# Kernel tuning notes

Measured on AMD Instinct MI355X. Metric: run time of the kernel, lower is better.

Reference implementation:

```python
import jax, jax.numpy as jnp
import numpy as np
import math

B, S, D, H = 2, 2048, 2048, 16
HD = D // H  # 128


def setup_inputs() -> dict:
    key = jax.random.key(0)
    ks = jax.random.split(key, 6)
    x = jax.random.normal(ks[0], (B, S, D), dtype=jnp.float32)
    scale = 1.0 / math.sqrt(D)
    wq = jax.random.normal(ks[1], (D, D), dtype=jnp.float32) * scale
    wk = jax.random.normal(ks[2], (D, D), dtype=jnp.float32) * scale
    wv = jax.random.normal(ks[3], (D, D), dtype=jnp.float32) * scale
    wo = jax.random.normal(ks[4], (D, D), dtype=jnp.float32) * scale
    # rotary frequencies: freqs_cis[t, j] = exp(i * t / theta^(2j/HD))
    theta = 10000.0
    inv = 1.0 / (theta ** (jnp.arange(0, HD, 2, dtype=jnp.float32) / HD))  # [HD//2]
    ang = jnp.arange(S, dtype=jnp.float32)[:, None] * inv[None, :]  # [S, HD//2]
    freqs_cos = jnp.cos(ang)
    freqs_sin = jnp.sin(ang)
    # causal additive mask
    mask = jnp.where(jnp.tril(jnp.ones((S, S), dtype=bool)), 0.0, -1e9)
    mask = mask[None, None, :, :].astype(jnp.float32)
    return {"x": x, "wq": wq, "wk": wk, "wv": wv, "wo": wo,
            "freqs_cos": freqs_cos, "freqs_sin": freqs_sin, "mask": mask}


def _rope(t, cos, sin):
    # t: [B, S, H, HD]; cos/sin: [S, HD//2]
    b, s, h, d = t.shape
    t2 = t.reshape(b, s, h, d // 2, 2)
    re, im = t2[..., 0], t2[..., 1]
    c = cos[None, :, None, :]
    sn = sin[None, :, None, :]
    out_re = re * c - im * sn
    out_im = re * sn + im * c
    return jnp.stack([out_re, out_im], axis=-1).reshape(b, s, h, d)


def reference(x, wq, wk, wv, wo, freqs_cos, freqs_sin, mask):
    b, s, _ = x.shape
    xq = (x @ wq.T).reshape(b, s, H, HD)
    xk = (x @ wk.T).reshape(b, s, H, HD)
    xv = (x @ wv.T).reshape(b, s, H, HD)
    xq = _rope(xq, freqs_cos, freqs_sin)
    xk = _rope(xk, freqs_cos, freqs_sin)
    # [B, H, S, HD]
    q = xq.transpose(0, 2, 1, 3)
    k = xk.transpose(0, 2, 1, 3)
    v = xv.transpose(0, 2, 1, 3)
    scores = jnp.einsum("bhqd,bhkd->bhqk", q, k) / math.sqrt(HD)
    scores = scores + mask
    probs = jax.nn.softmax(scores.astype(jnp.float32), axis=-1).astype(q.dtype)
    out = jnp.einsum("bhqk,bhkd->bhqd", probs, v)
    out = out.transpose(0, 2, 1, 3).reshape(b, s, -1)
    return out @ wo.T
```

## Files before the change

### kernel.cpp

```cpp
#include <hip/hip_runtime.h>
#include <math.h>

#define BATCH 2
#define SEQ 2048
#define DMODEL 2048
#define NH 16
#define HD 128

typedef __bf16 bf16x8 __attribute__((ext_vector_type(8)));
typedef __bf16 bf16x4 __attribute__((ext_vector_type(4)));
typedef float f32x4 __attribute__((ext_vector_type(4)));
typedef float f32x16 __attribute__((ext_vector_type(16)));

#define GLL16(dst, src)                                                          \
  __builtin_amdgcn_global_load_lds(                                              \
      (const __attribute__((address_space(1))) void*)(src),                      \
      (__attribute__((address_space(3))) void*)(dst), 16, 0, 0)

__global__ __launch_bounds__(256) void split_fp32(const float* __restrict__ src,
                                                  __bf16* __restrict__ hi,
                                                  __bf16* __restrict__ lo) {
  const size_t i = (size_t)blockIdx.x * 256 + threadIdx.x;
  const float4 v = ((const float4*)src)[i];
  bf16x4 h, L;
  h[0] = (__bf16)v.x; h[1] = (__bf16)v.y; h[2] = (__bf16)v.z; h[3] = (__bf16)v.w;
  L[0] = (__bf16)(v.x - (float)h[0]);
  L[1] = (__bf16)(v.y - (float)h[1]);
  L[2] = (__bf16)(v.z - (float)h[2]);
  L[3] = (__bf16)(v.w - (float)h[3]);
  ((bf16x4*)hi)[i] = h;
  ((bf16x4*)lo)[i] = L;
}

template <int EMIT>
__global__ __launch_bounds__(512, 2) void gemm8(const __bf16* __restrict__ Ah,
                                                const __bf16* __restrict__ Al,
                                                const __bf16* __restrict__ Bh,
                                                const __bf16* __restrict__ Bl,
                                                void* __restrict__ Cout) {
  extern __shared__ char sm[];
  constexpr int NT = 96;
  const int tid = threadIdx.x;
  const int l = tid & 63, w = tid >> 6;
  const int lg = l >> 4, lm = l & 15;
  const int wr = w >> 1, wc = w & 1;

  const int bid = (int)blockIdx.x;
  const int X = bid & 7, sub = bid >> 3;
  const int mb = (X & 3) * 4 + (sub >> 3);
  const int nb = (X >> 2) * 8 + (sub & 7);
  const int m0 = mb * 256, n0 = nb * 128;

  const __bf16* segA[3] = {Ah, Al, Ah};
  const __bf16* segB[3] = {Bh, Bh, Bl};

  const int srow = l >> 3;
  const int co = ((l & 7) ^ srow) * 8;

  char* const Abuf = sm;
  char* const Bbuf = sm + 98304;

  auto stageB = [&](int tb) {
    char* bd = Bbuf + (tb & 1) * 16384;
    const __bf16* sb = segB[tb >> 5];
    const int kw = (tb & 31) * 64;
#pragma unroll
    for (int j = 0; j < 2; ++j)
      GLL16(bd + (w * 2 + j) * 1024,
            sb + (size_t)(n0 + (w * 2 + j) * 8 + srow) * 2048 + kw + co);
  };
  auto stageAu = [&](int ta, int slot, int u) {
    char* ad = Abuf + slot * 32768 + u * 16384;
    const __bf16* sa = segA[ta >> 5];
    const int kw = (ta & 31) * 64;
#pragma unroll
    for (int j = 0; j < 2; ++j)
      GLL16(ad + (w * 2 + j) * 1024,
            sa + (size_t)(m0 + u * 128 + (w * 2 + j) * 8 + srow) * 2048 + kw + co);
  };

  stageAu(0, 0, 0); stageAu(0, 0, 1);
  stageB(0);
  stageAu(1, 1, 0); stageAu(1, 1, 1);

  f32x4 acc[4][4];
#pragma unroll
  for (int i = 0; i < 4; ++i)
#pragma unroll
    for (int j = 0; j < 4; ++j) { f32x4 z = {0.f, 0.f, 0.f, 0.f}; acc[i][j] = z; }

  int sA = 0, sA2 = 2;
  const int swz = lm & 7;

  for (int t = 0; t < NT; ++t) {
    if (t + 1 < NT) { asm volatile("s_waitcnt vmcnt(4)" ::: "memory"); }
    else            { asm volatile("s_waitcnt vmcnt(0)" ::: "memory"); }
    __builtin_amdgcn_sched_barrier(0);
    __builtin_amdgcn_s_barrier();

    const char* Ab = Abuf + sA * 32768;
    const char* Bb = Bbuf + (t & 1) * 16384;
    bf16x8 a[4], b[4];

#pragma unroll
    for (int j = 0; j < 4; ++j)
      b[j] = *(const bf16x8*)(Bb + (wc * 64 + j * 16 + lm) * 128 + ((lg ^ swz) << 4));
#pragma unroll
    for (int i = 0; i < 4; ++i)
      a[i] = *(const bf16x8*)(Ab + (wr * 64 + i * 16 + lm) * 128 + ((lg ^ swz) << 4));
    if (t + 1 < NT) stageB(t + 1);
    if (t + 2 < NT) stageAu(t + 2, sA2, 0);
    __builtin_amdgcn_s_barrier();
    __builtin_amdgcn_s_setprio(1);
#pragma unroll
    for (int i = 0; i < 4; ++i)
#pragma unroll
      for (int j = 0; j < 4; ++j)
        acc[i][j] = __builtin_amdgcn_mfma_f32_16x16x32_bf16(a[i], b[j], acc[i][j], 0, 0, 0);
    __builtin_amdgcn_s_setprio(0);

#pragma unroll
    for (int j = 0; j < 4; ++j)
      b[j] = *(const bf16x8*)(Bb + (wc * 64 + j * 16 + lm) * 128 + (((4 + lg) ^ swz) << 4));
#pragma unroll
    for (int i = 0; i < 4; ++i)
      a[i] = *(const bf16x8*)(Ab + (wr * 64 + i * 16 + lm) * 128 + (((4 + lg) ^ swz) << 4));
    if (t + 2 < NT) stageAu(t + 2, sA2, 1);
    __builtin_amdgcn_s_barrier();
    __builtin_amdgcn_s_setprio(1);
#pragma unroll
    for (int i = 0; i < 4; ++i)
#pragma unroll
      for (int j = 0; j < 4; ++j)
        acc[i][j] = __builtin_amdgcn_mfma_f32_16x16x32_bf16(a[i], b[j], acc[i][j], 0, 0, 0);
    __builtin_amdgcn_s_setprio(0);

    sA = (sA == 2) ? 0 : sA + 1;
    sA2 = (sA2 == 2) ? 0 : sA2 + 1;
  }

#pragma unroll
  for (int i = 0; i < 4; ++i)
#pragma unroll
    for (int j = 0; j < 4; ++j)
#pragma unroll
      for (int r = 0; r < 4; ++r) {
        const size_t row = (size_t)(m0 + wr * 64 + i * 16 + lg * 4 + r);
        const size_t col = (size_t)(n0 + wc * 64 + j * 16 + lm);
        if (EMIT == 0) ((float*)Cout)[row * 2048 + col] = acc[i][j][r];
        else           ((__bf16*)Cout)[row * 2048 + col] = (__bf16)acc[i][j][r];
      }
}

__global__ __launch_bounds__(256) void rope_bf16(__bf16* __restrict__ q,
                                                 __bf16* __restrict__ k,
                                                 const float* __restrict__ cosp,
                                                 const float* __restrict__ sinp) {
  __bf16* t = blockIdx.y ? k : q;
  const float scale = blockIdx.y ? 1.0f : 0.08838834764831845f;
  const size_t i4 = (size_t)blockIdx.x * 256 + threadIdx.x;
  const size_t e = i4 * 4;
  const int srow = (int)((e >> 11) & 2047);
  const int p = (int)(e & 127) >> 1;
  bf16x4 vv = *(bf16x4*)(t + e);
  const float c0 = cosp[srow * 64 + p],     s0 = sinp[srow * 64 + p];
  const float c1 = cosp[srow * 64 + p + 1], s1 = sinp[srow * 64 + p + 1];
  const float re0 = (float)vv[0], im0 = (float)vv[1];
  const float re1 = (float)vv[2], im1 = (float)vv[3];
  bf16x4 o;
  o[0] = (__bf16)((re0 * c0 - im0 * s0) * scale);
  o[1] = (__bf16)((re0 * s0 + im0 * c0) * scale);
  o[2] = (__bf16)((re1 * c1 - im1 * s1) * scale);
  o[3] = (__bf16)((re1 * s1 + im1 * c1) * scale);
  *(bf16x4*)(t + e) = o;
}

static __device__ __forceinline__ unsigned pk2(float a, float b) {
  unsigned short x = __builtin_bit_cast(unsigned short, (__bf16)a);
  unsigned short y = __builtin_bit_cast(unsigned short, (__bf16)b);
  return ((unsigned)y << 16) | (unsigned)x;
}

__global__ __launch_bounds__(256) void attn_mfma2(const __bf16* __restrict__ q,
                                                  const __bf16* __restrict__ k,
                                                  const __bf16* __restrict__ v,
                                                  __bf16* __restrict__ oh,
                                                  __bf16* __restrict__ ol) {
  __shared__ __align__(16) char Ks[64 * 272];
  __shared__ __align__(16) char Vt[128 * 144];

  const int tid = threadIdx.x;
  const int l = tid & 63, w = tid >> 6;
  const int l31 = l & 31, hg = l >> 5;

  const int f = (int)blockIdx.x;
  const int X = f & 7, t = f >> 3;
  const int g = X * 4 + (t & 3);
  const int qt = 15 - (t >> 2);
  const int b = g >> 4, h = g & 15;
  const int q0 = qt * 128;
  const size_t bh = (size_t)b * SEQ * DMODEL + (size_t)h * HD;

  bf16x8 qf[8];
  {
    const __bf16* qr = q + bh + (size_t)(q0 + 32 * w + l31) * DMODEL;
#pragma unroll
    for (int ks = 0; ks < 8; ++ks) qf[ks] = *(const bf16x8*)(qr + ks * 16 + hg * 8);
  }

  f32x16 accO[4];
#pragma unroll
  for (int dt = 0; dt < 4; ++dt)
#pragma unroll
    for (int i = 0; i < 16; ++i) accO[dt][i] = 0.f;
  float m_own = -1e30f, l_own = 0.f;

  const int srT = tid >> 4;
  const int scT = tid & 15;
  const int nkt = 2 * qt + 2;
  const int qg_own = q0 + 32 * w + l31;
  const int qg_min = q0 + 32 * w;

  bf16x8 kst[4], vst[4];
#pragma unroll
  for (int rnd = 0; rnd < 4; ++rnd) {
    const int r = srT + 16 * rnd;
    const size_t ga = bh + (size_t)(r) * DMODEL + scT * 8;
    kst[rnd] = *(const bf16x8*)(k + ga);
    vst[rnd] = *(const bf16x8*)(v + ga);
  }

  for (int kt = 0; kt < nkt; ++kt) {
    const int k0 = kt * 64;
    __syncthreads();
#pragma unroll
    for (int rnd = 0; rnd < 4; ++rnd) {
      const int r = srT + 16 * rnd;
      *(bf16x8*)(Ks + r * 272 + ((scT * 16) ^ (((r >> 3) & 7) << 4))) = kst[rnd];
      const int swz = (scT & 7) << 4;
      const int cb = (2 * r) ^ swz;
#pragma unroll
      for (int e = 0; e < 8; ++e)
        *(__bf16*)(Vt + (scT * 8 + e) * 144 + cb) = vst[rnd][e];
    }
    __syncthreads();
    if (kt + 1 < nkt) {
#pragma unroll
      for (int rnd = 0; rnd < 4; ++rnd) {
        const int r = srT + 16 * rnd;
        const size_t ga = bh + (size_t)((kt + 1) * 64 + r) * DMODEL + scT * 8;
        kst[rnd] = *(const bf16x8*)(k + ga);
        vst[rnd] = *(const bf16x8*)(v + ga);
      }
    }
    if (k0 > qg_min + 31) continue;

    f32x16 sc[2];
#pragma unroll
    for (int mt = 0; mt < 2; ++mt)
#pragma unroll
      for (int i = 0; i < 16; ++i) sc[mt][i] = 0.f;
#pragma unroll
    for (int mt = 0; mt < 2; ++mt) {
      const int row = mt * 32 + l31;
      const char* kr = Ks + row * 272;
      const int sx = ((row >> 3) & 7) << 4;
#pragma unroll
      for (int ks = 0; ks < 8; ++ks) {
        bf16x8 kf = *(const bf16x8*)(kr + ((ks * 32 + hg * 16) ^ sx));
        sc[mt] = __builtin_amdgcn_mfma_f32_32x32x16_bf16(kf, qf[ks], sc[mt], 0, 0, 0);
      }
    }

    if (k0 + 63 > qg_min) {
#pragma unroll
      for (int mt = 0; mt < 2; ++mt)
#pragma unroll
        for (int ri = 0; ri < 16; ++ri) {
          const int kg = k0 + mt * 32 + (ri & 3) + 8 * (ri >> 2) + 4 * hg;
          if (kg > qg_own) sc[mt][ri] = -INFINITY;
        }
    }

    float tm = -INFINITY;
#pragma unroll
    for (int mt = 0; mt < 2; ++mt)
#pragma unroll
      for (int ri = 0; ri < 16; ++ri) tm = fmaxf(tm, sc[mt][ri]);
    tm = fmaxf(tm, __shfl_xor(tm, 32));

    if (__any(tm > m_own)) {
      const float mnew = fmaxf(m_own, tm);
      const float alpha = __expf(m_own - mnew);
      m_own = mnew;
      l_own *= alpha;
#pragma unroll
      for (int ri = 0; ri < 16; ++ri) {
        const float a = __shfl(alpha, (ri & 3) + 8 * (ri >> 2) + 4 * hg);
#pragma unroll
        for (int dt = 0; dt < 4; ++dt) accO[dt][ri] *= a;
      }
    }
    float rs = 0.f;
#pragma unroll
    for (int mt = 0; mt < 2; ++mt)
#pragma unroll
      for (int ri = 0; ri < 16; ++ri) {
        const float p = __expf(sc[mt][ri] - m_own);
        sc[mt][ri] = p;
        rs += p;
      }
    rs += __shfl_xor(rs, 32);
    l_own += rs;

#pragma unroll
    for (int kk = 0; kk < 4; ++kk) {
      const int mt = kk >> 1, J8 = (kk & 1) * 8;
      unsigned oL0 = pk2(sc[mt][J8 + 0], sc[mt][J8 + 1]);
      unsigned oL1 = pk2(sc[mt][J8 + 2], sc[mt][J8 + 3]);
      unsigned oH0 = pk2(sc[mt][J8 + 4], sc[mt][J8 + 5]);
      unsigned oH1 = pk2(sc[mt][J8 + 6], sc[mt][J8 + 7]);
      unsigned s0 = hg ? oL0 : oH0;
      unsigned s1 = hg ? oL1 : oH1;
      const unsigned r0 = (unsigned)__shfl_xor((int)s0, 32);
      const unsigned r1 = (unsigned)__shfl_xor((int)s1, 32);
      int4 fi;
      fi.x = (int)(hg ? r0 : oL0);
      fi.y = (int)(hg ? r1 : oL1);
      fi.z = (int)(hg ? oH0 : r0);
      fi.w = (int)(hg ? oH1 : r1);
      const bf16x8 pa = __builtin_bit_cast(bf16x8, fi);
      const int kb = (kk * 32 + hg * 16);
#pragma unroll
      for (int dt = 0; dt < 4; ++dt) {
        const int d = dt * 32 + l31;
        bf16x8 vf = *(const bf16x8*)(Vt + d * 144 + (kb ^ (((d >> 3) & 7) << 4)));
        accO[dt] = __builtin_amdgcn_mfma_f32_32x32x16_bf16(pa, vf, accO[dt], 0, 0, 0);
      }
    }
  }

  const float inv_own = 1.f / l_own;
#pragma unroll
  for (int ri = 0; ri < 16; ++ri) {
    const int row = (ri & 3) + 8 * (ri >> 2) + 4 * hg;
    const float il = __shfl(inv_own, row & 31);
    const size_t rbase = bh + (size_t)(q0 + 32 * w + row) * DMODEL;
#pragma unroll
    for (int dt = 0; dt < 4; ++dt) {
      const float val = accO[dt][ri] * il;
      const size_t idx = rbase + dt * 32 + l31;
      const __bf16 hv = (__bf16)val;
      oh[idx] = hv;
      ol[idx] = (__bf16)(val - (float)hv);
    }
  }
}

extern "C" void kernel_launch(void* const* d_in, const int* in_sizes, int n_in,
                              void* d_out, int out_size, void* d_ws, size_t ws_size,
                              hipStream_t stream) {
  const float* x  = (const float*)d_in[0];
  const float* wq = (const float*)d_in[1];
  const float* wk = (const float*)d_in[2];
  const float* wv = (const float*)d_in[3];
  const float* wo = (const float*)d_in[4];
  const float* fc = (const float*)d_in[5];
  const float* fs = (const float*)d_in[6];

  const size_t NTOK = (size_t)BATCH * SEQ;
  const size_t NE   = NTOK * DMODEL;

  char* wsb = (char*)d_ws;
  __bf16* xh = (__bf16*)wsb;
  __bf16* xl = xh + NE;
  __bf16* wh = (__bf16*)(wsb + 2 * NE * 2);
  __bf16* wl = wh + (size_t)DMODEL * DMODEL;
  __bf16* vb = (__bf16*)(wsb + 2 * NE * 2 + 2 * (size_t)DMODEL * DMODEL * 2);
  __bf16* oh = xh;
  __bf16* ol = xl;
  __bf16* qb = (__bf16*)d_out;
  __bf16* kb = qb + NE;

  const int sx = (int)(NE / 4 / 256);
  const int sw = DMODEL * DMODEL / 4 / 256;
  const int SMEM = 131072;

  (void)hipFuncSetAttribute((const void*)gemm8<1>,
                            hipFuncAttributeMaxDynamicSharedMemorySize, SMEM);
  (void)hipFuncSetAttribute((const void*)gemm8<0>,
                            hipFuncAttributeMaxDynamicSharedMemorySize, SMEM);

  split_fp32<<<sx, 256, 0, stream>>>(x, xh, xl);

  split_fp32<<<sw, 256, 0, stream>>>(wq, wh, wl);
  gemm8<1><<<256, 512, SMEM, stream>>>(xh, xl, wh, wl, qb);
  split_fp32<<<sw, 256, 0, stream>>>(wk, wh, wl);
  gemm8<1><<<256, 512, SMEM, stream>>>(xh, xl, wh, wl, kb);
  split_fp32<<<sw, 256, 0, stream>>>(wv, wh, wl);
  gemm8<1><<<256, 512, SMEM, stream>>>(xh, xl, wh, wl, vb);

  rope_bf16<<<dim3(sx, 2), 256, 0, stream>>>(qb, kb, fc, fs);

  attn_mfma2<<<dim3(512), 256, 0, stream>>>(qb, kb, vb, oh, ol);

  split_fp32<<<sw, 256, 0, stream>>>(wo, wh, wl);
  gemm8<0><<<256, 512, SMEM, stream>>>(oh, ol, wh, wl, (float*)d_out);
}
```

Baseline: 651.1 us.

## Restructure split-bf16 GEMM to 4 waves with 128x64 warp tiles and K=32 stages

The projection GEMM moves from 512 threads (8 waves, 64x64 per wave, K-step 64 split into two halves) to 256 threads (4 waves, each computing a 128x64 tile) with a K-step of 32 per stage and half the LDS (64 KB). The LDS swizzle is changed to match 64-byte rows. The goal is more MFMA work per LDS fragment load and a smaller shared-memory footprint, which could allow more blocks per CU. The cost is double the accumulator registers per thread and twice as many pipeline iterations and barriers, and the vmcnt(4) wait is left as it was while stageA now issues 4 loads and stageB 2.

```diff
diff --git a/kernel.cpp b/kernel.cpp
--- a/kernel.cpp
+++ b/kernel.cpp
@@ -33,13 +33,13 @@
 }
 
 template <int EMIT>
-__global__ __launch_bounds__(512, 2) void gemm8(const __bf16* __restrict__ Ah,
+__global__ __launch_bounds__(256, 2) void gemm9(const __bf16* __restrict__ Ah,
                                                 const __bf16* __restrict__ Al,
                                                 const __bf16* __restrict__ Bh,
                                                 const __bf16* __restrict__ Bl,
                                                 void* __restrict__ Cout) {
   extern __shared__ char sm[];
-  constexpr int NT = 96;
+  constexpr int NT = 192;
   const int tid = threadIdx.x;
   const int l = tid & 63, w = tid >> 6;
   const int lg = l >> 4, lm = l & 15;
@@ -54,43 +54,43 @@
   const __bf16* segA[3] = {Ah, Al, Ah};
   const __bf16* segB[3] = {Bh, Bh, Bl};
 
-  const int srow = l >> 3;
-  const int co = ((l & 7) ^ srow) * 8;
+  const int sr = l >> 2;
+  const int co = ((l & 3) ^ ((l >> 3) & 3)) * 8;
 
   char* const Abuf = sm;
-  char* const Bbuf = sm + 98304;
-
-  auto stageB = [&](int tb) {
-    char* bd = Bbuf + (tb & 1) * 16384;
-    const __bf16* sb = segB[tb >> 5];
-    const int kw = (tb & 31) * 64;
+  char* const Bbuf = sm + 49152;
+
+  auto stageA = [&](int t, int slot) {
+    char* ad = Abuf + slot * 16384;
+    const __bf16* sa = segA[t >> 6];
+    const int kw = (t & 63) * 32;
+#pragma unroll
+    for (int j = 0; j < 4; ++j)
+      GLL16(ad + (w * 4 + j) * 1024,
+            sa + (size_t)(m0 + (w * 4 + j) * 16 + sr) * 2048 + kw + co);
+  };
+  auto stageB = [&](int t) {
+    char* bd = Bbuf + (t & 1) * 8192;
+    const __bf16* sb = segB[t >> 6];
+    const int kw = (t & 63) * 32;
 #pragma unroll
     for (int j = 0; j < 2; ++j)
       GLL16(bd + (w * 2 + j) * 1024,
-            sb + (size_t)(n0 + (w * 2 + j) * 8 + srow) * 2048 + kw + co);
+            sb + (size_t)(n0 + (w * 2 + j) * 16 + sr) * 2048 + kw + co);
   };
-  auto stageAu = [&](int ta, int slot, int u) {
-    char* ad = Abuf + slot * 32768 + u * 16384;
-    const __bf16* sa = segA[ta >> 5];
-    const int kw = (ta & 31) * 64;
-#pragma unroll
-    for (int j = 0; j < 2; ++j)
-      GLL16(ad + (w * 2 + j) * 1024,
-            sa + (size_t)(m0 + u * 128 + (w * 2 + j) * 8 + srow) * 2048 + kw + co);
-  };
-
-  stageAu(0, 0, 0); stageAu(0, 0, 1);
+
+  stageA(0, 0);
   stageB(0);
-  stageAu(1, 1, 0); stageAu(1, 1, 1);
-
-  f32x4 acc[4][4];
-#pragma unroll
-  for (int i = 0; i < 4; ++i)
+  stageA(1, 1);
+
+  f32x4 acc[8][4];
+#pragma unroll
+  for (int i = 0; i < 8; ++i)
 #pragma unroll
     for (int j = 0; j < 4; ++j) { f32x4 z = {0.f, 0.f, 0.f, 0.f}; acc[i][j] = z; }
 
   int sA = 0, sA2 = 2;
-  const int swz = lm & 7;
+  const int csw = (lm >> 1) & 3;
 
   for (int t = 0; t < NT; ++t) {
     if (t + 1 < NT) { asm volatile("s_waitcnt vmcnt(4)" ::: "memory"); }
@@ -98,54 +98,38 @@
     __builtin_amdgcn_sched_barrier(0);
     __builtin_amdgcn_s_barrier();
 
-    const char* Ab = Abuf + sA * 32768;
-    const char* Bb = Bbuf + (t & 1) * 16384;
-    bf16x8 a[4], b[4];
-
+    const char* Ab = Abuf + sA * 16384;
+    const char* Bb = Bbuf + (t & 1) * 8192;
+    bf16x8 a[8], b[4];
 #pragma unroll
     for (int j = 0; j < 4; ++j)
-      b[j] = *(const bf16x8*)(Bb + (wc * 64 + j * 16 + lm) * 128 + ((lg ^ swz) << 4));
-#pragma unroll
-    for (int i = 0; i < 4; ++i)
-      a[i] = *(const bf16x8*)(Ab + (wr * 64 + i * 16 + lm) * 128 + ((lg ^ swz) << 4));
+      b[j] = *(const bf16x8*)(Bb + (wc * 64 + j * 16 + lm) * 64 + ((lg ^ csw) << 4));
+#pragma unroll
+    for (int i = 0; i < 8; ++i)
+      a[i] = *(const bf16x8*)(Ab + (wr * 128 + i * 16 + lm) * 64 + ((lg ^ csw) << 4));
     if (t + 1 < NT) stageB(t + 1);
-    if (t + 2 < NT) stageAu(t + 2, sA2, 0);
+    if (t + 2 < NT) stageA(t + 2, sA2);
     __builtin_amdgcn_s_barrier();
+
     __builtin_amdgcn_s_setprio(1);
 #pragma unroll
-    for (int i = 0; i < 4; ++i)
+    for (int i = 0; i < 8; ++i)
 #pragma unroll
       for (int j = 0; j < 4; ++j)
         acc[i][j] = __builtin_amdgcn_mfma_f32_16x16x32_bf16(a[i], b[j], acc[i][j], 0, 0, 0);
     __builtin_amdgcn_s_setprio(0);
 
-#pragma unroll
-    for (int j = 0; j < 4; ++j)
-      b[j] = *(const bf16x8*)(Bb + (wc * 64 + j * 16 + lm) * 128 + (((4 + lg) ^ swz) << 4));
-#pragma unroll
-    for (int i = 0; i < 4; ++i)
-      a[i] = *(const bf16x8*)(Ab + (wr * 64 + i * 16 + lm) * 128 + (((4 + lg) ^ swz) << 4));
-    if (t + 2 < NT) stageAu(t + 2, sA2, 1);
-    __builtin_amdgcn_s_barrier();
-    __builtin_amdgcn_s_setprio(1);
-#pragma unroll
-    for (int i = 0; i < 4; ++i)
-#pragma unroll
-      for (int j = 0; j < 4; ++j)
-        acc[i][j] = __builtin_amdgcn_mfma_f32_16x16x32_bf16(a[i], b[j], acc[i][j], 0, 0, 0);
-    __builtin_amdgcn_s_setprio(0);
-
     sA = (sA == 2) ? 0 : sA + 1;
     sA2 = (sA2 == 2) ? 0 : sA2 + 1;
   }
 
 #pragma unroll
-  for (int i = 0; i < 4; ++i)
+  for (int i = 0; i < 8; ++i)
 #pragma unroll
     for (int j = 0; j < 4; ++j)
 #pragma unroll
       for (int r = 0; r < 4; ++r) {
-        const size_t row = (size_t)(m0 + wr * 64 + i * 16 + lg * 4 + r);
+        const size_t row = (size_t)(m0 + wr * 128 + i * 16 + lg * 4 + r);
         const size_t col = (size_t)(n0 + wc * 64 + j * 16 + lm);
         if (EMIT == 0) ((float*)Cout)[row * 2048 + col] = acc[i][j][r];
         else           ((__bf16*)Cout)[row * 2048 + col] = (__bf16)acc[i][j][r];
@@ -384,26 +368,26 @@
 
   const int sx = (int)(NE / 4 / 256);
   const int sw = DMODEL * DMODEL / 4 / 256;
-  const int SMEM = 131072;
-
-  (void)hipFuncSetAttribute((const void*)gemm8<1>,
+  const int SMEM = 65536;
+
+  (void)hipFuncSetAttribute((const void*)gemm9<1>,
                             hipFuncAttributeMaxDynamicSharedMemorySize, SMEM);
-  (void)hipFuncSetAttribute((const void*)gemm8<0>,
+  (void)hipFuncSetAttribute((const void*)gemm9<0>,
                             hipFuncAttributeMaxDynamicSharedMemorySize, SMEM);
 
   split_fp32<<<sx, 256, 0, stream>>>(x, xh, xl);
 
   split_fp32<<<sw, 256, 0, stream>>>(wq, wh, wl);
-  gemm8<1><<<256, 512, SMEM, stream>>>(xh, xl, wh, wl, qb);
+  gemm9<1><<<256, 256, SMEM, stream>>>(xh, xl, wh, wl, qb);
   split_fp32<<<sw, 256, 0, stream>>>(wk, wh, wl);
-  gemm8<1><<<256, 512, SMEM, stream>>>(xh, xl, wh, wl, kb);
+  gemm9<1><<<256, 256, SMEM, stream>>>(xh, xl, wh, wl, kb);
   split_fp32<<<sw, 256, 0, stream>>>(wv, wh, wl);
-  gemm8<1><<<256, 512, SMEM, stream>>>(xh, xl, wh, wl, vb);
+  gemm9<1><<<256, 256, SMEM, stream>>>(xh, xl, wh, wl, vb);
 
   rope_bf16<<<dim3(sx, 2), 256, 0, stream>>>(qb, kb, fc, fs);
 
   attn_mfma2<<<dim3(512), 256, 0, stream>>>(qb, kb, vb, oh, ol);
 
   split_fp32<<<sw, 256, 0, stream>>>(wo, wh, wl);
-  gemm8<0><<<256, 512, SMEM, stream>>>(oh, ol, wh, wl, (float*)d_out);
-}
+  gemm9<0><<<256, 256, SMEM, stream>>>(oh, ol, wh, wl, (float*)d_out);
+}
```

New measurement: 718.0 us. 10.3% more time.
